# Performance work log

Measured on AMD Instinct MI355X. Metric: run time of the kernel, lower is better.

## Reference

```python
import jax, jax.numpy as jnp
import numpy as np

B, S, D, H, L, DFF, NI, AD = 8, 512, 512, 8, 4, 2048, 20000, 128
DK = D // H


def _make_pe(max_len, d):
    pos = np.arange(max_len, dtype=np.float32)[:, None]
    div = np.exp(np.arange(0, d, 2, dtype=np.float32) * (-np.log(10000.0) / d))
    pe = np.zeros((max_len, d), dtype=np.float32)
    pe[:, 0::2] = np.sin(pos * div)
    pe[:, 1::2] = np.cos(pos * div)
    return jnp.asarray(pe)


def setup_inputs() -> dict:
    key = jax.random.key(0)
    ks = iter(jax.random.split(key, 64))
    def nrm(shape):
        return jax.random.normal(next(ks), shape, jnp.float32) * 0.02
    inp = {
        'item_ids': jax.random.randint(next(ks), (B, S), 0, NI),
        'audio_features': jax.random.normal(next(ks), (B, S, AD), jnp.float32),
        'is_organic': jax.random.bernoulli(next(ks), 0.5, (B, S)).astype(jnp.float32),
        'padding_mask': jnp.ones((B, 1, 1, S), jnp.float32),
        'emb_table': nrm((NI + 1, D)),
        'pe': _make_pe(S, D),
        'Wa1': nrm((AD, D)), 'ba1': jnp.zeros((D,)),
        'Wa2': nrm((D, D)), 'ba2': jnp.zeros((D,)),
        'Wf': nrm((2 * D, D)), 'bf': jnp.zeros((D,)),
        'Wq': nrm((L, D, D)), 'bq': jnp.zeros((L, D)),
        'Wk': nrm((L, D, D)), 'bk': jnp.zeros((L, D)),
        'Wv': nrm((L, D, D)), 'bv': jnp.zeros((L, D)),
        'Wo': nrm((L, D, D)), 'bo': jnp.zeros((L, D)),
        'worg': nrm((L, H)), 'borg': jnp.zeros((L, H)),
        'ln1s': jnp.ones((L, D)), 'ln1b': jnp.zeros((L, D)),
        'ln2s': jnp.ones((L, D)), 'ln2b': jnp.zeros((L, D)),
        'Wff1': nrm((L, D, DFF)), 'bff1': jnp.zeros((L, DFF)),
        'Wff2': nrm((L, DFF, D)), 'bff2': jnp.zeros((L, D)),
        'lnOs': jnp.ones((D,)), 'lnOb': jnp.zeros((D,)),
        'Wg': nrm((D + 1, D)), 'bg': jnp.zeros((D,)),
        'Wout': nrm((D, NI)), 'bout': jnp.zeros((NI,)),
    }
    return inp


def _ln(x, s, b, eps=1e-5):
    m = jnp.mean(x, -1, keepdims=True)
    v = jnp.mean((x - m) ** 2, -1, keepdims=True)
    return (x - m) * jax.lax.rsqrt(v + eps) * s + b


def reference(item_ids, audio_features, is_organic, padding_mask, emb_table, pe,
              Wa1, ba1, Wa2, ba2, Wf, bf, Wq, bq, Wk, bk, Wv, bv, Wo, bo,
              worg, borg, ln1s, ln1b, ln2s, ln2b, Wff1, bff1, Wff2, bff2,
              lnOs, lnOb, Wg, bg, Wout, bout):
    b_, s_ = item_ids.shape
    scale = 1.0 / np.sqrt(DK).astype(np.float32)
    tbl = emb_table.at[0].set(0.0)  # padding_idx=0
    item_emb = tbl[item_ids]                                    # (B,S,D)
    audio_emb = jax.nn.relu(audio_features @ Wa1 + ba1) @ Wa2 + ba2
    x = jax.nn.relu(jnp.concatenate([item_emb, audio_emb], -1) @ Wf + bf)
    x = x + pe[:s_]
    for l in range(L):
        q = (x @ Wq[l] + bq[l]).reshape(b_, s_, H, DK).transpose(0, 2, 1, 3)
        k = (x @ Wk[l] + bk[l]).reshape(b_, s_, H, DK).transpose(0, 2, 1, 3)
        v = (x @ Wv[l] + bv[l]).reshape(b_, s_, H, DK).transpose(0, 2, 1, 3)
        scores = jnp.einsum('bhqd,bhkd->bhqk', q, k) * scale    # (B,H,S,S)
        org = is_organic[:, :, None] * worg[l] + borg[l]        # (B,S,H)
        scores = scores + org.transpose(0, 2, 1)[..., None]     # per-query bias
        scores = jnp.where(padding_mask == 0, -1e9, scores)
        attn = jax.nn.softmax(scores, -1)
        ctx = jnp.einsum('bhqk,bhkd->bhqd', attn, v)
        ctx = ctx.transpose(0, 2, 1, 3).reshape(b_, s_, D)
        x = _ln(x + ctx @ Wo[l] + bo[l], ln1s[l], ln1b[l])
        ff = jax.nn.relu(x @ Wff1[l] + bff1[l]) @ Wff2[l] + bff2[l]
        x = _ln(x + ff, ln2s[l], ln2b[l])
    x = _ln(x, lnOs, lnOb)
    gate = jax.nn.sigmoid(jnp.concatenate([x, is_organic[..., None]], -1) @ Wg + bg)
    logits = (x * gate) @ Wout + bout                           # (B,S,NI)
    return logits
```

## Files before the change

kernel.cpp:

```cpp
#include <hip/hip_runtime.h>
#include <hip/hip_bf16.h>

typedef float f32x4 __attribute__((ext_vector_type(4)));
typedef __bf16 bf16x8 __attribute__((ext_vector_type(8)));

#define DEV __device__ __forceinline__

constexpr int B_ = 8, S_ = 512, D_ = 512, H_ = 8, L_ = 4, DFF_ = 2048, NI_ = 20000, AD_ = 128, DK_ = 64;
constexpr int N_ = B_ * S_;
constexpr int NOUT_PAD = 20096;

DEV void gload_lds16(const void* g, void* l) {
  __builtin_amdgcn_global_load_lds((const __attribute__((address_space(1))) unsigned int*)g,
                                   (__attribute__((address_space(3))) unsigned int*)l, 16, 0, 0);
}
DEV void gload_lds16_nt(const void* g, void* l) {
  __builtin_amdgcn_global_load_lds((const __attribute__((address_space(1))) unsigned int*)g,
                                   (__attribute__((address_space(3))) unsigned int*)l, 16, 0, 2);
}

DEV int xcd_swizzle(int bid, int nwg) {
  int q = nwg >> 3, r = nwg & 7;
  int x = bid & 7, idx = bid >> 3;
  int base = (x < r) ? x * (q + 1) : r * (q + 1) + (x - r) * q;
  return base + idx;
}

template<int NTB>
__global__ __launch_bounds__(512)
void gemm_big(const __hip_bfloat16* __restrict__ A, int lda,
              const __hip_bfloat16* __restrict__ Bm, int ldb,
              float* __restrict__ C, int ldc,
              const float* __restrict__ bias, int K, int Ncols)
{
  __shared__ __align__(16) unsigned short smA[2][256 * 32];
  __shared__ __align__(16) unsigned short smB[2][128 * 32];

  const int nwg = gridDim.x * gridDim.y;
  const int bid = blockIdx.y * gridDim.x + blockIdx.x;
  const int wgid = xcd_swizzle(bid, nwg);
  const int m0 = (wgid % gridDim.x) * 256, n0 = (wgid / gridDim.x) * 128;

  const int tid = threadIdx.x, wv = tid >> 6, lane = tid & 63;
  const int l15 = lane & 15, l4 = lane >> 4;
  const int wm = (wv >> 1) * 64, wn = (wv & 1) * 64;

  auto stage = [&](int buf, int k0) {
#pragma unroll
    for (int it = 0; it < 2; ++it) {
      int idx = it * 512 + tid, row = idx >> 2, c = idx & 3;
      int sc = c ^ ((row >> 1) & 3);
      gload_lds16((const void*)(A + (size_t)(m0 + row) * lda + k0 + sc * 8),
                  (void*)&smA[buf][(size_t)(it * 512 + wv * 64) * 8]);
    }
    {
      int row = tid >> 2, c = tid & 3;
      int sc = c ^ ((row >> 1) & 3);
      const void* src = (const void*)(Bm + (size_t)(n0 + row) * ldb + k0 + sc * 8);
      void* dst = (void*)&smB[buf][(size_t)(wv * 64) * 8];
      if constexpr (NTB) gload_lds16_nt(src, dst);
      else gload_lds16(src, dst);
    }
  };

  f32x4 acc[4][4];
#pragma unroll
  for (int i = 0; i < 4; ++i)
#pragma unroll
    for (int j = 0; j < 4; ++j) acc[i][j] = f32x4{0.f, 0.f, 0.f, 0.f};

  const int nk = K / 32;
  stage(0, 0);
  __syncthreads();

  int cur = 0;
  for (int t = 0; t < nk; ++t) {
    if (t + 1 < nk) stage(cur ^ 1, (t + 1) * 32);

    bf16x8 af[4], bfr[4];
#pragma unroll
    for (int i = 0; i < 4; ++i) {
      int row = wm + i * 16 + l15;
      int ch = l4 ^ ((row >> 1) & 3);
      af[i] = *reinterpret_cast<const bf16x8*>(&smA[cur][row * 32 + ch * 8]);
    }
#pragma unroll
    for (int j = 0; j < 4; ++j) {
      int row = wn + j * 16 + l15;
      int ch = l4 ^ ((row >> 1) & 3);
      bfr[j] = *reinterpret_cast<const bf16x8*>(&smB[cur][row * 32 + ch * 8]);
    }
    __builtin_amdgcn_s_setprio(1);
#pragma unroll
    for (int i = 0; i < 4; ++i)
#pragma unroll
      for (int j = 0; j < 4; ++j)
        acc[i][j] = __builtin_amdgcn_mfma_f32_16x16x32_bf16(af[i], bfr[j], acc[i][j], 0, 0, 0);
    __builtin_amdgcn_s_setprio(0);
    __syncthreads();
    cur ^= 1;
  }

#pragma unroll
  for (int i = 0; i < 4; ++i) {
#pragma unroll
    for (int j = 0; j < 4; ++j) {
#pragma unroll
      for (int r = 0; r < 4; ++r) {
        int row = m0 + wm + i * 16 + l4 * 4 + r;
        int col = n0 + wn + j * 16 + l15;
        if (col < Ncols) {
          float v = acc[i][j][r] + bias[col];
          __builtin_nontemporal_store(v, &C[(size_t)row * ldc + col]);
        }
      }
    }
  }
}

template<int BM, int BN, int EPI, int ACT, int NT>
__global__ __launch_bounds__(256)
void gemm2(const __hip_bfloat16* __restrict__ A, int lda,
           const __hip_bfloat16* __restrict__ Bm, int ldb,
           void* __restrict__ Cv, int ldc,
           const float* __restrict__ bias,
           const void* __restrict__ p1, const void* __restrict__ p2,
           const void* __restrict__ p3,
           int K, int Ncols)
{
  constexpr int BK = 64;
  constexpr int MI = BM / 32, NJ = BN / 32;
  constexpr int LA = BM * BK / 2048, LB = BN * BK / 2048;
  __shared__ __align__(16) unsigned short smA[2][BM * BK];
  __shared__ __align__(16) unsigned short smB[2][BN * BK];

  const int nwg = gridDim.x * gridDim.y;
  const int bid = blockIdx.y * gridDim.x + blockIdx.x;
  const int wgid = xcd_swizzle(bid, nwg);
  const int m0 = (wgid % gridDim.x) * BM, n0 = (wgid / gridDim.x) * BN;

  const int tid = threadIdx.x, wv = tid >> 6, lane = tid & 63;
  const int l15 = lane & 15, l4 = lane >> 4;
  const int wm = (wv >> 1) * (BM / 2), wn = (wv & 1) * (BN / 2);

  auto stage = [&](int buf, int k0) {
#pragma unroll
    for (int it = 0; it < LA; ++it) {
      int idx = it * 256 + tid, row = idx >> 3, c = idx & 7;
      int sc = c ^ (row & 7);
      gload_lds16((const void*)(A + (size_t)(m0 + row) * lda + k0 + sc * 8),
                  (void*)&smA[buf][(size_t)(it * 256 + wv * 64) * 8]);
    }
#pragma unroll
    for (int it = 0; it < LB; ++it) {
      int idx = it * 256 + tid, row = idx >> 3, c = idx & 7;
      int sc = c ^ (row & 7);
      gload_lds16((const void*)(Bm + (size_t)(n0 + row) * ldb + k0 + sc * 8),
                  (void*)&smB[buf][(size_t)(it * 256 + wv * 64) * 8]);
    }
  };

  f32x4 acc[MI][NJ];
#pragma unroll
  for (int i = 0; i < MI; ++i)
#pragma unroll
    for (int j = 0; j < NJ; ++j) acc[i][j] = f32x4{0.f, 0.f, 0.f, 0.f};

  const int nk = K / BK;
  stage(0, 0);
  __syncthreads();

  int cur = 0;
  for (int t = 0; t < nk; ++t) {
    if (t + 1 < nk) stage(cur ^ 1, (t + 1) * BK);

    bf16x8 af[MI][2], bfr[NJ][2];
#pragma unroll
    for (int i = 0; i < MI; ++i)
#pragma unroll
      for (int kk = 0; kk < 2; ++kk) {
        int row = wm + i * 16 + l15;
        int ch = (kk * 4 + l4) ^ (row & 7);
        af[i][kk] = *reinterpret_cast<const bf16x8*>(&smA[cur][row * BK + ch * 8]);
      }
#pragma unroll
    for (int j = 0; j < NJ; ++j)
#pragma unroll
      for (int kk = 0; kk < 2; ++kk) {
        int row = wn + j * 16 + l15;
        int ch = (kk * 4 + l4) ^ (row & 7);
        bfr[j][kk] = *reinterpret_cast<const bf16x8*>(&smB[cur][row * BK + ch * 8]);
      }
    __builtin_amdgcn_s_setprio(1);
#pragma unroll
    for (int kk = 0; kk < 2; ++kk)
#pragma unroll
      for (int i = 0; i < MI; ++i)
#pragma unroll
        for (int j = 0; j < NJ; ++j)
          acc[i][j] = __builtin_amdgcn_mfma_f32_16x16x32_bf16(af[i][kk], bfr[j][kk], acc[i][j], 0, 0, 0);
    __builtin_amdgcn_s_setprio(0);
    __syncthreads();
    cur ^= 1;
  }

#pragma unroll
  for (int i = 0; i < MI; ++i) {
#pragma unroll
    for (int j = 0; j < NJ; ++j) {
#pragma unroll
      for (int r = 0; r < 4; ++r) {
        int row = m0 + wm + i * 16 + l4 * 4 + r;
        int col = n0 + wn + j * 16 + l15;
        if (col < Ncols) {
          float v = acc[i][j][r];
          if (bias) v += bias[col];
          if (ACT == 1) v = v > 0.f ? v : 0.f;
          if constexpr (EPI == 0) {
            float* dst = &((float*)Cv)[(size_t)row * ldc + col];
            if constexpr (NT) __builtin_nontemporal_store(v, dst);
            else *dst = v;
          } else if constexpr (EPI == 1) {
            ((__hip_bfloat16*)Cv)[(size_t)row * ldc + col] = __float2bfloat16(v);
          } else if constexpr (EPI == 2) {
            v += ((const float*)p2)[(size_t)(row & 511) * 512 + col];
            ((float*)Cv)[(size_t)row * ldc + col] = v;
            ((__hip_bfloat16*)p1)[(size_t)row * ldc + col] = __float2bfloat16(v);
          } else if constexpr (EPI == 3) {
            if (col < 1024) {
              ((__hip_bfloat16*)Cv)[(size_t)(col >> 9) * N_ * 512 + (size_t)row * 512 + (col & 511)] =
                  __float2bfloat16(v);
            } else {
              int hd = col - 1024, b = row >> 9, s = row & 511;
              ((__hip_bfloat16*)p1)[((size_t)(b * 8 + (hd >> 6)) * 64 + (hd & 63)) * 512 + s] =
                  __float2bfloat16(v);
            }
          } else if constexpr (EPI == 4) {
            float zz = v + ((const float*)p2)[row] * ((const float*)p3)[col];
            float sg = 1.f / (1.f + __expf(-zz));
            float xn = ((const float*)p1)[(size_t)row * 512 + col];
            ((__hip_bfloat16*)Cv)[(size_t)row * 512 + col] = __float2bfloat16(xn * sg);
          }
        }
      }
    }
  }
}

__global__ __launch_bounds__(256)
void k_flash(const __hip_bfloat16* __restrict__ q, const __hip_bfloat16* __restrict__ k,
             const __hip_bfloat16* __restrict__ vt, const float* __restrict__ mask,
             __hip_bfloat16* __restrict__ ctx)
{
  __shared__ __align__(16) unsigned short Ql[64 * 64];
  __shared__ __align__(16) unsigned short Kl[2][64 * 64];
  __shared__ __align__(16) unsigned short Vl[2][64 * 64];
  __shared__ __align__(16) unsigned short Pl[4][16 * 64];

  const int qt = blockIdx.x, bh = blockIdx.y;
  const int b = bh >> 3, h = bh & 7;
  const int tid = threadIdx.x, wv = tid >> 6, lane = tid & 63;
  const int l15 = lane & 15, l4 = lane >> 4;
  const int q0 = qt * 64;

  const __hip_bfloat16* Qg = q + ((size_t)(b * 512 + q0) * 512) + h * 64;
  const __hip_bfloat16* Kg = k + ((size_t)(b * 512) * 512) + h * 64;
  const __hip_bfloat16* Vg = vt + ((size_t)bh * 64) * 512;
  const float* mk = mask + b * 512;

  auto stageQ = [&]() {
#pragma unroll
    for (int it = 0; it < 2; ++it) {
      int idx = it * 256 + wv * 64 + lane;
      int row = idx >> 3, c = idx & 7;
      gload_lds16((const void*)(Qg + (size_t)row * 512 + (c ^ (row & 7)) * 8),
                  (void*)&Ql[(it * 256 + wv * 64) * 8]);
    }
  };
  auto stageKV = [&](int buf, int kv0) {
#pragma unroll
    for (int it = 0; it < 2; ++it) {
      int idx = it * 256 + wv * 64 + lane;
      int row = idx >> 3, c = idx & 7;
      gload_lds16((const void*)(Kg + (size_t)(kv0 + row) * 512 + (c ^ (row & 7)) * 8),
                  (void*)&Kl[buf][(it * 256 + wv * 64) * 8]);
    }
#pragma unroll
    for (int it = 0; it < 2; ++it) {
      int idx = it * 256 + wv * 64 + lane;
      int row = idx >> 3, c = idx & 7;
      gload_lds16((const void*)(Vg + (size_t)row * 512 + kv0 + (c ^ (row & 7)) * 8),
                  (void*)&Vl[buf][(it * 256 + wv * 64) * 8]);
    }
  };

  stageQ();
  stageKV(0, 0);
  __syncthreads();

  bf16x8 aq[2];
#pragma unroll
  for (int kk = 0; kk < 2; ++kk) {
    int row = wv * 16 + l15;
    aq[kk] = *reinterpret_cast<const bf16x8*>(
        &Ql[row * 64 + (((kk * 4 + l4) ^ (row & 7)) * 8)]);
  }

  f32x4 accO[4];
  float mrun[4], lrun[4];
#pragma unroll
  for (int j = 0; j < 4; ++j) accO[j] = f32x4{0.f, 0.f, 0.f, 0.f};
#pragma unroll
  for (int r = 0; r < 4; ++r) { mrun[r] = -3e38f; lrun[r] = 0.f; }

  int cur = 0;
  for (int t = 0; t < 8; ++t) {
    if (t + 1 < 8) stageKV(cur ^ 1, (t + 1) * 64);
    const int kv0 = t * 64;

    f32x4 s[4];
#pragma unroll
    for (int j = 0; j < 4; ++j) s[j] = f32x4{0.f, 0.f, 0.f, 0.f};
#pragma unroll
    for (int kk = 0; kk < 2; ++kk) {
#pragma unroll
      for (int j = 0; j < 4; ++j) {
        int row = j * 16 + l15;
        bf16x8 bk = *reinterpret_cast<const bf16x8*>(
            &Kl[cur][row * 64 + (((kk * 4 + l4) ^ (row & 7)) * 8)]);
        s[j] = __builtin_amdgcn_mfma_f32_16x16x32_bf16(aq[kk], bk, s[j], 0, 0, 0);
      }
    }

#pragma unroll
    for (int j = 0; j < 4; ++j) {
      float mval = mk[kv0 + j * 16 + l15];
#pragma unroll
      for (int r = 0; r < 4; ++r)
        s[j][r] = (mval == 0.f) ? -1e30f : s[j][r];
    }

    float alpha[4];
#pragma unroll
    for (int r = 0; r < 4; ++r) {
      float v = fmaxf(fmaxf(s[0][r], s[1][r]), fmaxf(s[2][r], s[3][r]));
      v = fmaxf(v, __shfl_xor(v, 1));
      v = fmaxf(v, __shfl_xor(v, 2));
      v = fmaxf(v, __shfl_xor(v, 4));
      v = fmaxf(v, __shfl_xor(v, 8));
      float mn = fmaxf(mrun[r], v);
      alpha[r] = __expf(mrun[r] - mn);
      mrun[r] = mn;
    }
    float rs[4] = {0.f, 0.f, 0.f, 0.f};
#pragma unroll
    for (int j = 0; j < 4; ++j)
#pragma unroll
      for (int r = 0; r < 4; ++r) {
        float p = __expf(s[j][r] - mrun[r]);
        s[j][r] = p;
        rs[r] += p;
      }
#pragma unroll
    for (int r = 0; r < 4; ++r) {
      float v = rs[r];
      v += __shfl_xor(v, 1); v += __shfl_xor(v, 2);
      v += __shfl_xor(v, 4); v += __shfl_xor(v, 8);
      lrun[r] = lrun[r] * alpha[r] + v;
#pragma unroll
      for (int j = 0; j < 4; ++j) accO[j][r] *= alpha[r];
    }

#pragma unroll
    for (int j = 0; j < 4; ++j)
#pragma unroll
      for (int r = 0; r < 4; ++r) {
        int qrow = l4 * 4 + r, key = j * 16 + l15;
        __hip_bfloat16 hb = __float2bfloat16(s[j][r]);
        Pl[wv][qrow * 64 + (((key >> 3) ^ (qrow & 7)) * 8) + (key & 7)] =
            *reinterpret_cast<unsigned short*>(&hb);
      }

#pragma unroll
    for (int kc = 0; kc < 2; ++kc) {
      bf16x8 ap = *reinterpret_cast<const bf16x8*>(
          &Pl[wv][l15 * 64 + (((kc * 4 + l4) ^ (l15 & 7)) * 8)]);
#pragma unroll
      for (int j = 0; j < 4; ++j) {
        int row = j * 16 + l15;
        bf16x8 bv2 = *reinterpret_cast<const bf16x8*>(
            &Vl[cur][row * 64 + (((kc * 4 + l4) ^ (row & 7)) * 8)]);
        accO[j] = __builtin_amdgcn_mfma_f32_16x16x32_bf16(ap, bv2, accO[j], 0, 0, 0);
      }
    }
    __syncthreads();
    cur ^= 1;
  }

#pragma unroll
  for (int r = 0; r < 4; ++r) {
    float inv = lrun[r] > 0.f ? 1.f / lrun[r] : 0.f;
#pragma unroll
    for (int j = 0; j < 4; ++j) {
      int row = q0 + wv * 16 + l4 * 4 + r;
      int col = h * 64 + j * 16 + l15;
      ctx[(size_t)(b * 512 + row) * 512 + col] = __float2bfloat16(accO[j][r] * inv);
    }
  }
}

__global__ void k_transpose(const float* __restrict__ in, __hip_bfloat16* __restrict__ out,
                            int K, int N, long inBatch, long outBatch, float scale)
{
  __shared__ float tile[32][33];
  int z = blockIdx.z;
  const float* ip = in + (long)z * inBatch;
  __hip_bfloat16* op = out + (long)z * outBatch;
  int n0 = blockIdx.x * 32, k0 = blockIdx.y * 32;
  int tx = threadIdx.x, ty = threadIdx.y;
#pragma unroll
  for (int r = 0; r < 4; ++r) {
    int k = k0 + ty + r * 8, n = n0 + tx;
    if (k < K && n < N) tile[ty + r * 8][tx] = ip[(size_t)k * N + n];
  }
  __syncthreads();
#pragma unroll
  for (int r = 0; r < 4; ++r) {
    int n = n0 + ty + r * 8, k = k0 + tx;
    if (n < N && k < K) op[(size_t)n * K + k] = __float2bfloat16(tile[tx][ty + r * 8] * scale);
  }
}

__global__ void k_packbias(const float* __restrict__ bq, const float* __restrict__ bk,
                           const float* __restrict__ bv, float* __restrict__ out) {
  int i = blockIdx.x * 256 + threadIdx.x;
  int d = i & 511, t = (i >> 9) % 3, l = i / (3 * 512);
  const float* src = (t == 0) ? bq : (t == 1) ? bk : bv;
  out[i] = src[l * 512 + d] * (t == 0 ? 0.125f : 1.f);
}

__global__ void k_front(const int* __restrict__ ids, const float* __restrict__ tbl,
                        const float* __restrict__ audio,
                        __hip_bfloat16* __restrict__ cat, __hip_bfloat16* __restrict__ ab) {
  int n = blockIdx.x, t = threadIdx.x;
  int id = ids[n];
  const float* src = tbl + (size_t)id * 512;
  size_t dst = (size_t)n * 1024;
  float a0 = (id == 0) ? 0.f : src[t];
  float a1 = (id == 0) ? 0.f : src[t + 256];
  cat[dst + t] = __float2bfloat16(a0);
  cat[dst + t + 256] = __float2bfloat16(a1);
  if (t < 128) ab[(size_t)n * 128 + t] = __float2bfloat16(audio[(size_t)n * 128 + t]);
}

__global__ void k_ln(const float* __restrict__ x, const float* __restrict__ y,
                     const float* __restrict__ gam, const float* __restrict__ bet,
                     float* __restrict__ xout, __hip_bfloat16* __restrict__ xb) {
  int row = blockIdx.x, t = threadIdx.x;
  size_t base = (size_t)row * 512;
  float v0 = x[base + t], v1 = x[base + t + 256];
  if (y) { v0 += y[base + t]; v1 += y[base + t + 256]; }
  __shared__ float sm[4];
  float s = v0 + v1;
  for (int o = 32; o; o >>= 1) s += __shfl_xor(s, o);
  if ((t & 63) == 0) sm[t >> 6] = s;
  __syncthreads();
  float mean = (sm[0] + sm[1] + sm[2] + sm[3]) * (1.f / 512.f);
  __syncthreads();
  float d0 = v0 - mean, d1 = v1 - mean;
  float qq = d0 * d0 + d1 * d1;
  for (int o = 32; o; o >>= 1) qq += __shfl_xor(qq, o);
  if ((t & 63) == 0) sm[t >> 6] = qq;
  __syncthreads();
  float var = (sm[0] + sm[1] + sm[2] + sm[3]) * (1.f / 512.f);
  float rs = rsqrtf(var + 1e-5f);
  float o0 = d0 * rs * gam[t] + bet[t];
  float o1 = d1 * rs * gam[t + 256] + bet[t + 256];
  xout[base + t] = o0;
  xout[base + t + 256] = o1;
  xb[base + t] = __float2bfloat16(o0);
  xb[base + t + 256] = __float2bfloat16(o1);
}

extern "C" void kernel_launch(void* const* d_in, const int* in_sizes, int n_in,
                              void* d_out, int out_size, void* d_ws, size_t ws_size,
                              hipStream_t stream) {
  typedef __hip_bfloat16 bf;
  const int*   item_ids = (const int*)  d_in[0];
  const float* audio    = (const float*)d_in[1];
  const float* organic  = (const float*)d_in[2];
  const float* mask     = (const float*)d_in[3];
  const float* emb      = (const float*)d_in[4];
  const float* pe       = (const float*)d_in[5];
  const float* Wa1 = (const float*)d_in[6],  *ba1 = (const float*)d_in[7];
  const float* Wa2 = (const float*)d_in[8],  *ba2 = (const float*)d_in[9];
  const float* Wf  = (const float*)d_in[10], *bfb = (const float*)d_in[11];
  const float* Wq  = (const float*)d_in[12], *bq  = (const float*)d_in[13];
  const float* Wk  = (const float*)d_in[14], *bk  = (const float*)d_in[15];
  const float* Wv  = (const float*)d_in[16], *bv  = (const float*)d_in[17];
  const float* Wo  = (const float*)d_in[18], *bo  = (const float*)d_in[19];
  const float* ln1s = (const float*)d_in[22], *ln1b = (const float*)d_in[23];
  const float* ln2s = (const float*)d_in[24], *ln2b = (const float*)d_in[25];
  const float* Wff1 = (const float*)d_in[26], *bff1 = (const float*)d_in[27];
  const float* Wff2 = (const float*)d_in[28], *bff2 = (const float*)d_in[29];
  const float* lnOs = (const float*)d_in[30], *lnOb = (const float*)d_in[31];
  const float* Wg   = (const float*)d_in[32], *bg   = (const float*)d_in[33];
  const float* Wout = (const float*)d_in[34], *bout = (const float*)d_in[35];
  float* out = (float*)d_out;

  char* ws = (char*)d_ws;
  size_t off = 0;
  auto alloc = [&](size_t bytes) -> char* {
    char* p = ws + off;
    off = (off + bytes + 255) & ~(size_t)255;
    return p;
  };
  bf* Wa1T = (bf*)alloc((size_t)512 * 128 * 2);
  bf* Wa2T = (bf*)alloc((size_t)512 * 512 * 2);
  bf* WfT  = (bf*)alloc((size_t)512 * 1024 * 2);
  bf* WqkvT = (bf*)alloc((size_t)L_ * 3 * D_ * D_ * 2);
  bf* WoT  = (bf*)alloc((size_t)L_ * D_ * D_ * 2);
  bf* Wff1T = (bf*)alloc((size_t)L_ * DFF_ * D_ * 2);
  bf* Wff2T = (bf*)alloc((size_t)L_ * D_ * DFF_ * 2);
  bf* WgT   = (bf*)alloc((size_t)512 * 512 * 2);
  bf* WoutT = (bf*)alloc((size_t)NOUT_PAD * 512 * 2);
  float* bqkv = (float*)alloc((size_t)L_ * 3 * 512 * 4);
  bf* ab    = (bf*)alloc((size_t)N_ * AD_ * 2);
  bf* cat   = (bf*)alloc((size_t)N_ * 1024 * 2);
  bf* ah    = (bf*)alloc((size_t)N_ * 512 * 2);
  float* xf = (float*)alloc((size_t)N_ * 512 * 4);
  bf* xb    = (bf*)alloc((size_t)N_ * 512 * 2);
  bf* qkv   = (bf*)alloc((size_t)3 * N_ * 512 * 2);
  bf* vt    = (bf*)alloc((size_t)B_ * H_ * DK_ * S_ * 2);
  bf* ctxb  = (bf*)alloc((size_t)N_ * 512 * 2);
  float* ybuf = (float*)alloc((size_t)N_ * 512 * 4);
  bf* ff1b  = (bf*)alloc((size_t)N_ * DFF_ * 2);
  bf* xg    = (bf*)alloc((size_t)N_ * 512 * 2);
  if (off > ws_size) return;

  bf* qb = qkv;
  bf* kb = qkv + (size_t)N_ * 512;

  dim3 tb(32, 8);
  k_transpose<<<dim3(16, 4, 1),  tb, 0, stream>>>(Wa1, Wa1T, 128, 512, 0, 0, 1.f);
  k_transpose<<<dim3(16, 16, 1), tb, 0, stream>>>(Wa2, Wa2T, 512, 512, 0, 0, 1.f);
  k_transpose<<<dim3(16, 32, 1), tb, 0, stream>>>(Wf, WfT, 1024, 512, 0, 0, 1.f);
  k_transpose<<<dim3(16, 16, L_), tb, 0, stream>>>(Wq, WqkvT, 512, 512,
      (long)D_ * D_, (long)3 * D_ * D_, 0.125f);
  k_transpose<<<dim3(16, 16, L_), tb, 0, stream>>>(Wk, WqkvT + (size_t)D_ * D_, 512, 512,
      (long)D_ * D_, (long)3 * D_ * D_, 1.f);
  k_transpose<<<dim3(16, 16, L_), tb, 0, stream>>>(Wv, WqkvT + (size_t)2 * D_ * D_, 512, 512,
      (long)D_ * D_, (long)3 * D_ * D_, 1.f);
  k_transpose<<<dim3(16, 16, L_), tb, 0, stream>>>(Wo, WoT, 512, 512, (long)D_ * D_, (long)D_ * D_, 1.f);
  k_transpose<<<dim3(64, 16, L_), tb, 0, stream>>>(Wff1, Wff1T, 512, 2048, (long)D_ * DFF_, (long)D_ * DFF_, 1.f);
  k_transpose<<<dim3(16, 64, L_), tb, 0, stream>>>(Wff2, Wff2T, 2048, 512, (long)DFF_ * D_, (long)DFF_ * D_, 1.f);
  k_transpose<<<dim3(16, 16, 1), tb, 0, stream>>>(Wg, WgT, 512, 512, 0, 0, 1.f);
  k_transpose<<<dim3(625, 16, 1), tb, 0, stream>>>(Wout, WoutT, 512, 20000, 0, 0, 1.f);
  k_packbias<<<(L_ * 3 * 512) / 256, 256, 0, stream>>>(bq, bk, bv, bqkv);

  k_front<<<N_, 256, 0, stream>>>(item_ids, emb, audio, cat, ab);
  gemm2<128, 64, 1, 1, 0><<<dim3(32, 8), 256, 0, stream>>>(ab, 128, Wa1T, 128,
      (void*)ah, 512, ba1, nullptr, nullptr, nullptr, 128, 512);
  gemm2<128, 64, 1, 0, 0><<<dim3(32, 8), 256, 0, stream>>>(ah, 512, Wa2T, 512,
      (void*)(cat + 512), 1024, ba2, nullptr, nullptr, nullptr, 512, 512);
  gemm2<128, 64, 2, 1, 0><<<dim3(32, 8), 256, 0, stream>>>(cat, 1024, WfT, 1024,
      (void*)xf, 512, bfb, (void*)xb, (const void*)pe, nullptr, 1024, 512);

  for (int l = 0; l < L_; ++l) {
    gemm2<128, 64, 3, 0, 0><<<dim3(32, 24), 256, 0, stream>>>(xb, 512,
        WqkvT + (size_t)l * 3 * D_ * D_, 512, (void*)qkv, 512,
        bqkv + (size_t)l * 3 * 512, (void*)vt, nullptr, nullptr, 512, 1536);
    k_flash<<<dim3(8, B_ * H_), 256, 0, stream>>>(qb, kb, vt, mask, ctxb);
    gemm2<128, 64, 0, 0, 0><<<dim3(32, 8), 256, 0, stream>>>(ctxb, 512,
        WoT + (size_t)l * D_ * D_, 512, (void*)ybuf, 512, bo + l * D_,
        nullptr, nullptr, nullptr, 512, 512);
    k_ln<<<N_, 256, 0, stream>>>(xf, ybuf, ln1s + l * D_, ln1b + l * D_, xf, xb);
    gemm2<128, 128, 1, 1, 0><<<dim3(32, 16), 256, 0, stream>>>(xb, 512,
        Wff1T + (size_t)l * DFF_ * D_, 512, (void*)ff1b, 2048, bff1 + l * DFF_,
        nullptr, nullptr, nullptr, 512, 2048);
    gemm2<128, 64, 0, 0, 0><<<dim3(32, 8), 256, 0, stream>>>(ff1b, 2048,
        Wff2T + (size_t)l * D_ * DFF_, 2048, (void*)ybuf, 512, bff2 + l * D_,
        nullptr, nullptr, nullptr, 2048, 512);
    k_ln<<<N_, 256, 0, stream>>>(xf, ybuf, ln2s + l * D_, ln2b + l * D_, xf, xb);
  }

  k_ln<<<N_, 256, 0, stream>>>(xf, nullptr, lnOs, lnOb, xf, xb);
  gemm2<128, 64, 4, 0, 0><<<dim3(32, 8), 256, 0, stream>>>(xb, 512, WgT, 512,
      (void*)xg, 512, bg, (const void*)xf, (const void*)organic,
      (const void*)(Wg + (size_t)512 * 512), 512, 512);
  gemm_big<1><<<dim3(16, 157), 512, 0, stream>>>(xg, 512, WoutT, 512,
      out, 20000, bout, 512, 20000);
}
```

Baseline: 906.3 us.

## Merge weight transposes into one launch, fuse residual add, drop nontemporal B loads

Combines the eleven weight-transpose launches and the bias-pack launch into a single kernel that dispatches work by block index. Adds a GEMM epilogue that adds the residual stream, so the Wo and FF2 GEMMs write x+y directly and layer norm reads one input instead of two. Also removes the nontemporal load hint on the B operand of the output-projection GEMM. This saves launch overhead and some memory traffic, at the cost of a large, branchy transpose kernel.

```diff
diff --git a/kernel.cpp b/kernel.cpp
--- a/kernel.cpp
+++ b/kernel.cpp
@@ -13,10 +13,6 @@
 DEV void gload_lds16(const void* g, void* l) {
   __builtin_amdgcn_global_load_lds((const __attribute__((address_space(1))) unsigned int*)g,
                                    (__attribute__((address_space(3))) unsigned int*)l, 16, 0, 0);
-}
-DEV void gload_lds16_nt(const void* g, void* l) {
-  __builtin_amdgcn_global_load_lds((const __attribute__((address_space(1))) unsigned int*)g,
-                                   (__attribute__((address_space(3))) unsigned int*)l, 16, 0, 2);
 }
 
 DEV int xcd_swizzle(int bid, int nwg) {
@@ -26,7 +22,6 @@
   return base + idx;
 }
 
-template<int NTB>
 __global__ __launch_bounds__(512)
 void gemm_big(const __hip_bfloat16* __restrict__ A, int lda,
               const __hip_bfloat16* __restrict__ Bm, int ldb,
@@ -56,10 +51,8 @@
     {
       int row = tid >> 2, c = tid & 3;
       int sc = c ^ ((row >> 1) & 3);
-      const void* src = (const void*)(Bm + (size_t)(n0 + row) * ldb + k0 + sc * 8);
-      void* dst = (void*)&smB[buf][(size_t)(wv * 64) * 8];
-      if constexpr (NTB) gload_lds16_nt(src, dst);
-      else gload_lds16(src, dst);
+      gload_lds16((const void*)(Bm + (size_t)(n0 + row) * ldb + k0 + sc * 8),
+                  (void*)&smB[buf][(size_t)(wv * 64) * 8]);
     }
   };
 
@@ -240,6 +233,9 @@
             float sg = 1.f / (1.f + __expf(-zz));
             float xn = ((const float*)p1)[(size_t)row * 512 + col];
             ((__hip_bfloat16*)Cv)[(size_t)row * 512 + col] = __float2bfloat16(xn * sg);
+          } else if constexpr (EPI == 5) {
+            v += ((const float*)p2)[(size_t)row * 512 + col];
+            ((float*)Cv)[(size_t)row * ldc + col] = v;
           }
         }
       }
@@ -409,34 +405,65 @@
   }
 }
 
-__global__ void k_transpose(const float* __restrict__ in, __hip_bfloat16* __restrict__ out,
-                            int K, int N, long inBatch, long outBatch, float scale)
+__global__ __launch_bounds__(256)
+void k_trans_all(const float* __restrict__ Wa1, const float* __restrict__ Wa2,
+                 const float* __restrict__ Wf, const float* __restrict__ Wq,
+                 const float* __restrict__ Wk, const float* __restrict__ Wv,
+                 const float* __restrict__ Wo, const float* __restrict__ Wff1,
+                 const float* __restrict__ Wff2, const float* __restrict__ Wg,
+                 const float* __restrict__ Wout,
+                 const float* __restrict__ bq, const float* __restrict__ bk,
+                 const float* __restrict__ bv,
+                 __hip_bfloat16* Wa1T, __hip_bfloat16* Wa2T, __hip_bfloat16* WfT,
+                 __hip_bfloat16* WqkvT, __hip_bfloat16* WoT, __hip_bfloat16* Wff1T,
+                 __hip_bfloat16* Wff2T, __hip_bfloat16* WgT, __hip_bfloat16* WoutT,
+                 float* bqkv)
 {
   __shared__ float tile[32][33];
-  int z = blockIdx.z;
-  const float* ip = in + (long)z * inBatch;
-  __hip_bfloat16* op = out + (long)z * outBatch;
-  int n0 = blockIdx.x * 32, k0 = blockIdx.y * 32;
-  int tx = threadIdx.x, ty = threadIdx.y;
-#pragma unroll
-  for (int r = 0; r < 4; ++r) {
-    int k = k0 + ty + r * 8, n = n0 + tx;
-    if (k < K && n < N) tile[ty + r * 8][tx] = ip[(size_t)k * N + n];
-  }
-  __syncthreads();
-#pragma unroll
-  for (int r = 0; r < 4; ++r) {
-    int n = n0 + ty + r * 8, k = k0 + tx;
-    if (n < N && k < K) op[(size_t)n * K + k] = __float2bfloat16(tile[tx][ty + r * 8] * scale);
-  }
-}
-
-__global__ void k_packbias(const float* __restrict__ bq, const float* __restrict__ bk,
-                           const float* __restrict__ bv, float* __restrict__ out) {
-  int i = blockIdx.x * 256 + threadIdx.x;
-  int d = i & 511, t = (i >> 9) % 3, l = i / (3 * 512);
-  const float* src = (t == 0) ? bq : (t == 1) ? bk : bv;
-  out[i] = src[l * 512 + d] * (t == 0 ? 0.125f : 1.f);
+  const int bid = blockIdx.x, tid = threadIdx.x;
+  const int tx = tid & 31, ty = tid >> 5;
+
+  auto tr = [&](const float* ip, __hip_bfloat16* op, int K, int N, int NTX,
+                int t, float scale) {
+    int bx = t % NTX, by = t / NTX;
+    int n0 = bx * 32, k0 = by * 32;
+#pragma unroll
+    for (int r = 0; r < 4; ++r) {
+      int k = k0 + ty + r * 8, n = n0 + tx;
+      if (k < K && n < N) tile[ty + r * 8][tx] = ip[(size_t)k * N + n];
+    }
+    __syncthreads();
+#pragma unroll
+    for (int r = 0; r < 4; ++r) {
+      int n = n0 + ty + r * 8, k = k0 + tx;
+      if (n < N && k < K) op[(size_t)n * K + k] = __float2bfloat16(tile[tx][ty + r * 8] * scale);
+    }
+  };
+
+  constexpr int DD = 512 * 512, FD = 512 * 2048;
+  if (bid < 64)        tr(Wa1, Wa1T, 128, 512, 16, bid, 1.f);
+  else if (bid < 320)  tr(Wa2, Wa2T, 512, 512, 16, bid - 64, 1.f);
+  else if (bid < 832)  tr(Wf, WfT, 1024, 512, 16, bid - 320, 1.f);
+  else if (bid < 1856) { int rl = bid - 832,  z = rl >> 8;
+    tr(Wq + (size_t)z * DD, WqkvT + (size_t)z * 3 * DD, 512, 512, 16, rl & 255, 0.125f); }
+  else if (bid < 2880) { int rl = bid - 1856, z = rl >> 8;
+    tr(Wk + (size_t)z * DD, WqkvT + (size_t)z * 3 * DD + DD, 512, 512, 16, rl & 255, 1.f); }
+  else if (bid < 3904) { int rl = bid - 2880, z = rl >> 8;
+    tr(Wv + (size_t)z * DD, WqkvT + (size_t)z * 3 * DD + 2 * DD, 512, 512, 16, rl & 255, 1.f); }
+  else if (bid < 4928) { int rl = bid - 3904, z = rl >> 8;
+    tr(Wo + (size_t)z * DD, WoT + (size_t)z * DD, 512, 512, 16, rl & 255, 1.f); }
+  else if (bid < 9024) { int rl = bid - 4928, z = rl >> 10;
+    tr(Wff1 + (size_t)z * FD, Wff1T + (size_t)z * FD, 512, 2048, 64, rl & 1023, 1.f); }
+  else if (bid < 13120) { int rl = bid - 9024, z = rl >> 10;
+    tr(Wff2 + (size_t)z * FD, Wff2T + (size_t)z * FD, 2048, 512, 16, rl & 1023, 1.f); }
+  else if (bid < 13376) tr(Wg, WgT, 512, 512, 16, bid - 13120, 1.f);
+  else if (bid < 23376) tr(Wout, WoutT, 512, 20000, 625, bid - 13376, 1.f);
+  else {
+    int i = (bid - 23376) * 256 + tid;
+    int d = i & 511, t2 = (i >> 9) % 3, l = i / (3 * 512);
+    const float* src = (t2 == 0) ? bq : (t2 == 1) ? bk : bv;
+    bqkv[i] = src[l * 512 + d] * (t2 == 0 ? 0.125f : 1.f);
+  }
 }
 
 __global__ void k_front(const int* __restrict__ ids, const float* __restrict__ tbl,
@@ -541,22 +568,9 @@
   bf* qb = qkv;
   bf* kb = qkv + (size_t)N_ * 512;
 
-  dim3 tb(32, 8);
-  k_transpose<<<dim3(16, 4, 1),  tb, 0, stream>>>(Wa1, Wa1T, 128, 512, 0, 0, 1.f);
-  k_transpose<<<dim3(16, 16, 1), tb, 0, stream>>>(Wa2, Wa2T, 512, 512, 0, 0, 1.f);
-  k_transpose<<<dim3(16, 32, 1), tb, 0, stream>>>(Wf, WfT, 1024, 512, 0, 0, 1.f);
-  k_transpose<<<dim3(16, 16, L_), tb, 0, stream>>>(Wq, WqkvT, 512, 512,
-      (long)D_ * D_, (long)3 * D_ * D_, 0.125f);
-  k_transpose<<<dim3(16, 16, L_), tb, 0, stream>>>(Wk, WqkvT + (size_t)D_ * D_, 512, 512,
-      (long)D_ * D_, (long)3 * D_ * D_, 1.f);
-  k_transpose<<<dim3(16, 16, L_), tb, 0, stream>>>(Wv, WqkvT + (size_t)2 * D_ * D_, 512, 512,
-      (long)D_ * D_, (long)3 * D_ * D_, 1.f);
-  k_transpose<<<dim3(16, 16, L_), tb, 0, stream>>>(Wo, WoT, 512, 512, (long)D_ * D_, (long)D_ * D_, 1.f);
-  k_transpose<<<dim3(64, 16, L_), tb, 0, stream>>>(Wff1, Wff1T, 512, 2048, (long)D_ * DFF_, (long)D_ * DFF_, 1.f);
-  k_transpose<<<dim3(16, 64, L_), tb, 0, stream>>>(Wff2, Wff2T, 2048, 512, (long)DFF_ * D_, (long)DFF_ * D_, 1.f);
-  k_transpose<<<dim3(16, 16, 1), tb, 0, stream>>>(Wg, WgT, 512, 512, 0, 0, 1.f);
-  k_transpose<<<dim3(625, 16, 1), tb, 0, stream>>>(Wout, WoutT, 512, 20000, 0, 0, 1.f);
-  k_packbias<<<(L_ * 3 * 512) / 256, 256, 0, stream>>>(bq, bk, bv, bqkv);
+  k_trans_all<<<23400, 256, 0, stream>>>(Wa1, Wa2, Wf, Wq, Wk, Wv, Wo, Wff1, Wff2,
+      Wg, Wout, bq, bk, bv,
+      Wa1T, Wa2T, WfT, WqkvT, WoT, Wff1T, Wff2T, WgT, WoutT, bqkv);
 
   k_front<<<N_, 256, 0, stream>>>(item_ids, emb, audio, cat, ab);
   gemm2<128, 64, 1, 1, 0><<<dim3(32, 8), 256, 0, stream>>>(ab, 128, Wa1T, 128,
@@ -571,23 +585,23 @@
         WqkvT + (size_t)l * 3 * D_ * D_, 512, (void*)qkv, 512,
         bqkv + (size_t)l * 3 * 512, (void*)vt, nullptr, nullptr, 512, 1536);
     k_flash<<<dim3(8, B_ * H_), 256, 0, stream>>>(qb, kb, vt, mask, ctxb);
-    gemm2<128, 64, 0, 0, 0><<<dim3(32, 8), 256, 0, stream>>>(ctxb, 512,
+    gemm2<128, 64, 5, 0, 0><<<dim3(32, 8), 256, 0, stream>>>(ctxb, 512,
         WoT + (size_t)l * D_ * D_, 512, (void*)ybuf, 512, bo + l * D_,
-        nullptr, nullptr, nullptr, 512, 512);
-    k_ln<<<N_, 256, 0, stream>>>(xf, ybuf, ln1s + l * D_, ln1b + l * D_, xf, xb);
+        nullptr, (const void*)xf, nullptr, 512, 512);
+    k_ln<<<N_, 256, 0, stream>>>(ybuf, nullptr, ln1s + l * D_, ln1b + l * D_, xf, xb);
     gemm2<128, 128, 1, 1, 0><<<dim3(32, 16), 256, 0, stream>>>(xb, 512,
         Wff1T + (size_t)l * DFF_ * D_, 512, (void*)ff1b, 2048, bff1 + l * DFF_,
         nullptr, nullptr, nullptr, 512, 2048);
-    gemm2<128, 64, 0, 0, 0><<<dim3(32, 8), 256, 0, stream>>>(ff1b, 2048,
+    gemm2<128, 64, 5, 0, 0><<<dim3(32, 8), 256, 0, stream>>>(ff1b, 2048,
         Wff2T + (size_t)l * D_ * DFF_, 2048, (void*)ybuf, 512, bff2 + l * D_,
-        nullptr, nullptr, nullptr, 2048, 512);
-    k_ln<<<N_, 256, 0, stream>>>(xf, ybuf, ln2s + l * D_, ln2b + l * D_, xf, xb);
+        nullptr, (const void*)xf, nullptr, 2048, 512);
+    k_ln<<<N_, 256, 0, stream>>>(ybuf, nullptr, ln2s + l * D_, ln2b + l * D_, xf, xb);
   }
 
   k_ln<<<N_, 256, 0, stream>>>(xf, nullptr, lnOs, lnOb, xf, xb);
   gemm2<128, 64, 4, 0, 0><<<dim3(32, 8), 256, 0, stream>>>(xb, 512, WgT, 512,
       (void*)xg, 512, bg, (const void*)xf, (const void*)organic,
       (const void*)(Wg + (size_t)512 * 512), 512, 512);
-  gemm_big<1><<<dim3(16, 157), 512, 0, stream>>>(xg, 512, WoutT, 512,
+  gemm_big<<<dim3(16, 157), 512, 0, stream>>>(xg, 512, WoutT, 512,
       out, 20000, bout, 512, 20000);
 }
```

Result: faster. 871.5 us (-3.8%).
